# Optimization experiments

Measured on AMD Instinct MI355X. Metric: run time of the kernel, lower is better.

Reference implementation:

```python
import jax, jax.numpy as jnp
import numpy as np

N = 50000   # nodes
E = 1600000 # edges
C = 32      # all channel dims


def _p(k, shape):
    return jax.random.normal(k, shape, dtype=jnp.float32) * 0.05


def setup_inputs() -> dict:
    key = jax.random.key(0)
    ks = jax.random.split(key, 32)
    inp = {
        "node_attr": jax.random.normal(ks[0], (N, C), dtype=jnp.float32),
        "edge_attr": jax.random.normal(ks[1], (E, C), dtype=jnp.float32),
        "edge_index": jax.random.randint(ks[2], (2, E), 0, N, dtype=jnp.int32),
        # conv1: in = 2*32 + 32 = 96
        "c1w1": _p(ks[3], (96, C)),  "c1b1": jnp.zeros((C,), jnp.float32),
        "c1w2": _p(ks[4], (C, C)),   "c1b2": jnp.zeros((C,), jnp.float32),
        # conv2: in = 2*32 + 64 = 128
        "c2w1": _p(ks[5], (128, C)), "c2b1": jnp.zeros((C,), jnp.float32),
        "c2w2": _p(ks[6], (C, C)),   "c2b2": jnp.zeros((C,), jnp.float32),
        # conv3: in = 2*32 + 96 = 160
        "c3w1": _p(ks[7], (160, C)), "c3b1": jnp.zeros((C,), jnp.float32),
        "c3w2": _p(ks[8], (C, C)),   "c3b2": jnp.zeros((C,), jnp.float32),
        # node_out_mlp: three 32->32 linears
        "nw1": _p(ks[9], (C, C)),  "nb1": jnp.zeros((C,), jnp.float32),
        "nw2": _p(ks[10], (C, C)), "nb2": jnp.zeros((C,), jnp.float32),
        "nw3": _p(ks[11], (C, C)), "nb3": jnp.zeros((C,), jnp.float32),
        # edge_out_mlp: three 32->32 linears
        "ew1": _p(ks[12], (C, C)), "eb1": jnp.zeros((C,), jnp.float32),
        "ew2": _p(ks[13], (C, C)), "eb2": jnp.zeros((C,), jnp.float32),
        "ew3": _p(ks[14], (C, C)), "eb3": jnp.zeros((C,), jnp.float32),
    }
    return inp


def _lrelu(x):
    return jnp.where(x > 0, x, 0.2 * x)


def _edge_conv(x, row, col, ea, w1, b1, w2, b2):
    # gather endpoints, concat with edge features, 2-layer MLP on edges
    h = jnp.concatenate([x[row], x[col], ea], axis=1)        # [E, 2C + ce]
    edge_out = jax.nn.relu(h @ w1 + b1) @ w2 + b2            # [E, C]
    # scatter-mean back to source nodes (zero-degree nodes -> 0)
    n = x.shape[0]
    s = jax.ops.segment_sum(edge_out, row, num_segments=n)
    cnt = jax.ops.segment_sum(jnp.ones((edge_out.shape[0], 1), edge_out.dtype), row, num_segments=n)
    node_out = s / jnp.maximum(cnt, 1.0)
    return node_out, edge_out


def reference(node_attr, edge_attr, edge_index,
              c1w1, c1b1, c1w2, c1b2,
              c2w1, c2b1, c2w2, c2b2,
              c3w1, c3b1, c3w2, c3b2,
              nw1, nb1, nw2, nb2, nw3, nb3,
              ew1, eb1, ew2, eb2, ew3, eb3):
    row, col = edge_index[0], edge_index[1]

    n1, e1 = _edge_conv(node_attr, row, col, edge_attr, c1w1, c1b1, c1w2, c1b2)
    n1, e1 = _lrelu(n1), _lrelu(e1)

    n2, e2 = _edge_conv(n1, row, col, jnp.concatenate([e1, edge_attr], axis=-1),
                        c2w1, c2b1, c2w2, c2b2)
    n2, e2 = _lrelu(n2), _lrelu(e2)

    n3, e3 = _edge_conv(n2, row, col, jnp.concatenate([e2, e1, edge_attr], axis=-1),
                        c3w1, c3b1, c3w2, c3b2)
    n3, e3 = _lrelu(n3), _lrelu(e3)

    node_out = _lrelu(_lrelu(n3 @ nw1 + nb1) @ nw2 + nb2) @ nw3 + nb3
    edge_out = _lrelu(_lrelu(e3 @ ew1 + eb1) @ ew2 + eb2) @ ew3 + eb3
    return node_out, edge_out
```

## Files before the change

### kernel.cpp

```cpp
#include <hip/hip_runtime.h>

#define DEVINL __device__ __forceinline__

constexpr int PADF = 36;

DEVINL float lrelu1(float v)    { return v > 0.f ? v : 0.2f * v; }
DEVINL float invlrelu1(float v) { return v > 0.f ? v : 5.0f * v; }

DEVINL void gemm_block(const float* __restrict__ wg, const float* hrow, float acc[32])
{
#pragma unroll
    for (int cb = 0; cb < 4; ++cb) {
#pragma unroll 1
        for (int kq = 0; kq < 8; ++kq) {
            float4 h = *(const float4*)(hrow + kq * 4);
#pragma unroll
            for (int i = 0; i < 4; ++i) {
                float hv = ((const float*)&h)[i];
                float w8[8];
                *(float4*)&w8[0] = *(const float4*)(wg + (kq * 4 + i) * 32 + cb * 8);
                *(float4*)&w8[4] = *(const float4*)(wg + (kq * 4 + i) * 32 + cb * 8 + 4);
#pragma unroll
                for (int jj = 0; jj < 8; ++jj)
                    acc[cb * 8 + jj] = fmaf(hv, w8[jj], acc[cb * 8 + jj]);
            }
        }
    }
}

DEVINL void stage_rows(const float* __restrict__ src, float* __restrict__ hs,
                       int base, int se, int sq, int limit)
{
#pragma unroll
    for (int p = 0; p < 8; ++p) {
        int lr = p * 32 + se;
        int m = base + lr; if (m >= limit) m = limit - 1;
        float4 v = *(const float4*)(src + (size_t)m * 32 + sq * 4);
        *(float4*)&hs[lr * PADF + sq * 4] = v;
    }
}

__global__ __launch_bounds__(256)
void hist_kernel(const int* __restrict__ rowi, int* __restrict__ deg, int E)
{
    int e = blockIdx.x * 256 + threadIdx.x;
    if (e < E) atomicAdd(&deg[rowi[e]], 1);
}

__global__ __launch_bounds__(256)
void scan_kernel(const int* __restrict__ deg, int* __restrict__ off,
                 int* __restrict__ cursor, int N, int E)
{
    __shared__ int part[256];
    __shared__ int psum[256];
    const int t = threadIdx.x;
    const int per = (N + 255) / 256;
    const int b0 = t * per;
    int s = 0;
    for (int i = 0; i < per; ++i) { int idx = b0 + i; if (idx < N) s += deg[idx]; }
    part[t] = s;
    __syncthreads();
    if (t == 0) { int run = 0; for (int i = 0; i < 256; ++i) { psum[i] = run; run += part[i]; } }
    __syncthreads();
    int run = psum[t];
    for (int i = 0; i < per; ++i) {
        int idx = b0 + i;
        if (idx < N) { off[idx] = run; cursor[idx] = run; run += deg[idx]; }
    }
    if (t == 0) off[N] = E;
}

__global__ __launch_bounds__(256)
void place_kernel(const int* __restrict__ rowi, int* __restrict__ cursor,
                  int* __restrict__ perm, int E)
{
    int e = blockIdx.x * 256 + threadIdx.x;
    if (e < E) {
        int r = rowi[e];
        int p = atomicAdd(&cursor[r], 1);
        perm[p] = e;
    }
}

__global__ __launch_bounds__(256, 4)
void pre_kernel(const float* __restrict__ x, const float* __restrict__ w1,
                const float* __restrict__ b1,
                float* __restrict__ Pr, float* __restrict__ Pc, int N)
{
    __shared__ float hs[256 * PADF];
    const int tid = threadIdx.x;
    const int base = blockIdx.x * 256;
    const int se = tid >> 3, sq = tid & 7;
    const float* hrow = hs + tid * PADF;

    stage_rows(x, hs, base, se, sq, N);
    __syncthreads();

    const int n = base + tid;
    float acc[32];
#pragma unroll
    for (int j = 0; j < 32; ++j) acc[j] = b1[j];
    gemm_block(w1, hrow, acc);
    if (n < N) {
#pragma unroll
        for (int j = 0; j < 32; j += 4)
            *(float4*)(Pr + (size_t)n * 32 + j) = make_float4(acc[j], acc[j+1], acc[j+2], acc[j+3]);
    }
#pragma unroll
    for (int j = 0; j < 32; ++j) acc[j] = 0.f;
    gemm_block(w1 + 1024, hrow, acc);
    if (n < N) {
#pragma unroll
        for (int j = 0; j < 32; j += 4)
            *(float4*)(Pc + (size_t)n * 32 + j) = make_float4(acc[j], acc[j+1], acc[j+2], acc[j+3]);
    }
}

template<int NCHUNK, bool FUSE>
__global__ __launch_bounds__(256, 4)
void conv_kernel(const float* __restrict__ Pr, const float* __restrict__ Pc,
                 const int* __restrict__ rowi, const int* __restrict__ coli,
                 const float* __restrict__ f0, const float* __restrict__ f1,
                 const float* __restrict__ f2,
                 const float* __restrict__ w1e,
                 const float* __restrict__ w2g, const float* __restrict__ b2g,
                 float* __restrict__ eout,
                 const float* __restrict__ mw1, const float* __restrict__ mb1,
                 const float* __restrict__ mw2, const float* __restrict__ mb2,
                 const float* __restrict__ mw3, const float* __restrict__ mb3,
                 float* __restrict__ mout,
                 int E)
{
    __shared__ float hs[256 * PADF];
    const int tid = threadIdx.x;
    const int base = blockIdx.x * 256;
    const int se = tid >> 3, sq = tid & 7;
    float* hrow = hs + tid * PADF;

    stage_rows(f0, hs, base, se, sq, E);

    const int e = base + tid;
    const int ee = e < E ? e : E - 1;
    const int r = rowi[ee], c = coli[ee];
    const float* pr = Pr + (size_t)r * 32;
    const float* pc = Pc + (size_t)c * 32;
    float4 ga[8], gb[8];
#pragma unroll
    for (int q = 0; q < 8; ++q) ga[q] = *(const float4*)(pr + q * 4);
#pragma unroll
    for (int q = 0; q < 8; ++q) gb[q] = *(const float4*)(pc + q * 4);
    float acc[32];
#pragma unroll
    for (int q = 0; q < 8; ++q) {
        acc[q * 4 + 0] = ga[q].x + gb[q].x;
        acc[q * 4 + 1] = ga[q].y + gb[q].y;
        acc[q * 4 + 2] = ga[q].z + gb[q].z;
        acc[q * 4 + 3] = ga[q].w + gb[q].w;
    }

    __syncthreads();
    gemm_block(w1e, hrow, acc);
#pragma unroll
    for (int cch = 1; cch < NCHUNK; ++cch) {
        const float* src = (cch == 1) ? f1 : f2;
        __syncthreads();
        stage_rows(src, hs, base, se, sq, E);
        __syncthreads();
        gemm_block(w1e + cch * 1024, hrow, acc);
    }

#pragma unroll
    for (int j = 0; j < 32; j += 4) {
        float4 v;
        v.x = fmaxf(acc[j],     0.f); v.y = fmaxf(acc[j + 1], 0.f);
        v.z = fmaxf(acc[j + 2], 0.f); v.w = fmaxf(acc[j + 3], 0.f);
        *(float4*)&hrow[j] = v;
    }
    float acc2[32];
#pragma unroll
    for (int j = 0; j < 32; ++j) acc2[j] = b2g[j];
    gemm_block(w2g, hrow, acc2);

    if constexpr (!FUSE) {
        if (e < E) {
#pragma unroll
            for (int j = 0; j < 32; j += 4) {
                float4 v;
                v.x = lrelu1(acc2[j]);     v.y = lrelu1(acc2[j + 1]);
                v.z = lrelu1(acc2[j + 2]); v.w = lrelu1(acc2[j + 3]);
                *(float4*)(eout + (size_t)e * 32 + j) = v;
            }
        }
    } else {
#pragma unroll
        for (int j = 0; j < 32; j += 4) {
            float4 v;
            v.x = lrelu1(acc2[j]);     v.y = lrelu1(acc2[j + 1]);
            v.z = lrelu1(acc2[j + 2]); v.w = lrelu1(acc2[j + 3]);
            *(float4*)&hrow[j] = v;
            if (e < E) *(float4*)(eout + (size_t)e * 32 + j) = v;
        }
        float acc3[32];
#pragma unroll
        for (int j = 0; j < 32; ++j) acc3[j] = mb1[j];
        gemm_block(mw1, hrow, acc3);
#pragma unroll
        for (int j = 0; j < 32; j += 4) {
            float4 v;
            v.x = lrelu1(acc3[j]);     v.y = lrelu1(acc3[j + 1]);
            v.z = lrelu1(acc3[j + 2]); v.w = lrelu1(acc3[j + 3]);
            *(float4*)&hrow[j] = v;
        }
#pragma unroll
        for (int j = 0; j < 32; ++j) acc3[j] = mb2[j];
        gemm_block(mw2, hrow, acc3);
#pragma unroll
        for (int j = 0; j < 32; j += 4) {
            float4 v;
            v.x = lrelu1(acc3[j]);     v.y = lrelu1(acc3[j + 1]);
            v.z = lrelu1(acc3[j + 2]); v.w = lrelu1(acc3[j + 3]);
            *(float4*)&hrow[j] = v;
        }
#pragma unroll
        for (int j = 0; j < 32; ++j) acc3[j] = mb3[j];
        gemm_block(mw3, hrow, acc3);
        if (e < E) {
#pragma unroll
            for (int j = 0; j < 32; j += 4)
                *(float4*)(mout + (size_t)e * 32 + j) =
                    make_float4(acc3[j], acc3[j + 1], acc3[j + 2], acc3[j + 3]);
        }
    }
}

__global__ __launch_bounds__(256)
void mean_kernel(const float* __restrict__ esrc, const int* __restrict__ off,
                 const int* __restrict__ perm, float* __restrict__ nout, int N)
{
    const int t = threadIdx.x;
    const int n = blockIdx.x * 32 + (t >> 3);
    if (n >= N) return;
    const int cg = t & 7;
    const int o0 = off[n], o1 = off[n + 1];
    float4 acc = make_float4(0.f, 0.f, 0.f, 0.f);
    for (int i = o0; i < o1; ++i) {
        int e = perm[i];
        float4 v = *(const float4*)(esrc + (size_t)e * 32 + cg * 4);
        acc.x += invlrelu1(v.x); acc.y += invlrelu1(v.y);
        acc.z += invlrelu1(v.z); acc.w += invlrelu1(v.w);
    }
    float inv = 1.0f / (float)max(o1 - o0, 1);
    float4 r;
    r.x = lrelu1(acc.x * inv); r.y = lrelu1(acc.y * inv);
    r.z = lrelu1(acc.z * inv); r.w = lrelu1(acc.w * inv);
    *(float4*)(nout + (size_t)n * 32 + cg * 4) = r;
}

__global__ __launch_bounds__(256, 4)
void mlp3_kernel(const float* __restrict__ in,
                 const float* __restrict__ w1g, const float* __restrict__ b1g,
                 const float* __restrict__ w2g, const float* __restrict__ b2g,
                 const float* __restrict__ w3g, const float* __restrict__ b3g,
                 float* __restrict__ out, int M)
{
    __shared__ float hs[256 * PADF];
    const int tid = threadIdx.x;
    const int base = blockIdx.x * 256;
    const int se = tid >> 3, sq = tid & 7;
    float* hrow = hs + tid * PADF;

    stage_rows(in, hs, base, se, sq, M);
    __syncthreads();

    float acc[32];
#pragma unroll
    for (int j = 0; j < 32; ++j) acc[j] = b1g[j];
    gemm_block(w1g, hrow, acc);
#pragma unroll
    for (int j = 0; j < 32; j += 4) {
        float4 v;
        v.x = lrelu1(acc[j]);     v.y = lrelu1(acc[j + 1]);
        v.z = lrelu1(acc[j + 2]); v.w = lrelu1(acc[j + 3]);
        *(float4*)&hrow[j] = v;
    }
#pragma unroll
    for (int j = 0; j < 32; ++j) acc[j] = b2g[j];
    gemm_block(w2g, hrow, acc);
#pragma unroll
    for (int j = 0; j < 32; j += 4) {
        float4 v;
        v.x = lrelu1(acc[j]);     v.y = lrelu1(acc[j + 1]);
        v.z = lrelu1(acc[j + 2]); v.w = lrelu1(acc[j + 3]);
        *(float4*)&hrow[j] = v;
    }
#pragma unroll
    for (int j = 0; j < 32; ++j) acc[j] = b3g[j];
    gemm_block(w3g, hrow, acc);

    int m = base + tid;
    if (m < M) {
#pragma unroll
        for (int j = 0; j < 32; j += 4)
            *(float4*)(out + (size_t)m * 32 + j) =
                make_float4(acc[j], acc[j + 1], acc[j + 2], acc[j + 3]);
    }
}

extern "C" void kernel_launch(void* const* d_in, const int* in_sizes, int n_in,
                              void* d_out, int out_size, void* d_ws, size_t ws_size,
                              hipStream_t stream)
{
    const float* node_attr = (const float*)d_in[0];
    const float* edge_attr = (const float*)d_in[1];
    const int*   eidx      = (const int*)d_in[2];
    const float* c1w1 = (const float*)d_in[3];  const float* c1b1 = (const float*)d_in[4];
    const float* c1w2 = (const float*)d_in[5];  const float* c1b2 = (const float*)d_in[6];
    const float* c2w1 = (const float*)d_in[7];  const float* c2b1 = (const float*)d_in[8];
    const float* c2w2 = (const float*)d_in[9];  const float* c2b2 = (const float*)d_in[10];
    const float* c3w1 = (const float*)d_in[11]; const float* c3b1 = (const float*)d_in[12];
    const float* c3w2 = (const float*)d_in[13]; const float* c3b2 = (const float*)d_in[14];
    const float* nw1  = (const float*)d_in[15]; const float* nb1  = (const float*)d_in[16];
    const float* nw2  = (const float*)d_in[17]; const float* nb2  = (const float*)d_in[18];
    const float* nw3  = (const float*)d_in[19]; const float* nb3  = (const float*)d_in[20];
    const float* ew1  = (const float*)d_in[21]; const float* eb1  = (const float*)d_in[22];
    const float* ew2  = (const float*)d_in[23]; const float* eb2  = (const float*)d_in[24];
    const float* ew3  = (const float*)d_in[25]; const float* eb3  = (const float*)d_in[26];

    const int N = in_sizes[0] / 32;
    const int E = in_sizes[1] / 32;
    const int* rowi = eidx;
    const int* coli = eidx + E;

    float* out      = (float*)d_out;
    float* node_out = out;
    float* edge_out = out + (size_t)N * 32;

    int* deg    = (int*)d_ws;
    int* off    = deg + N;
    int* cursor = off + (N + 1);
    int* perm   = cursor + N;
    uintptr_t a = ((uintptr_t)(perm + E) + 255) & ~(uintptr_t)255;
    float* n1 = (float*)a;
    float* n2 = n1 + (size_t)32 * N;
    float* e1 = n2 + (size_t)32 * N;
    float* e2 = e1 + (size_t)32 * E;

    const int gridE   = (E + 255) / 256;
    const int gridN32 = (N + 31) / 32;
    const int gridN   = (N + 255) / 256;

    hipMemsetAsync(deg, 0, (size_t)N * sizeof(int), stream);
    hist_kernel<<<gridE, 256, 0, stream>>>(rowi, deg, E);
    scan_kernel<<<1, 256, 0, stream>>>(deg, off, cursor, N, E);
    place_kernel<<<gridE, 256, 0, stream>>>(rowi, cursor, perm, E);

    pre_kernel<<<gridN, 256, 0, stream>>>(node_attr, c1w1, c1b1, n1, n2, N);
    conv_kernel<1, false><<<gridE, 256, 0, stream>>>(
        n1, n2, rowi, coli, edge_attr, nullptr, nullptr,
        c1w1 + 2048, c1w2, c1b2, e1,
        nullptr, nullptr, nullptr, nullptr, nullptr, nullptr, nullptr, E);
    mean_kernel<<<gridN32, 256, 0, stream>>>(e1, off, perm, n1, N);

    pre_kernel<<<gridN, 256, 0, stream>>>(n1, c2w1, c2b1, n1, n2, N);
    conv_kernel<2, false><<<gridE, 256, 0, stream>>>(
        n1, n2, rowi, coli, e1, edge_attr, nullptr,
        c2w1 + 2048, c2w2, c2b2, e2,
        nullptr, nullptr, nullptr, nullptr, nullptr, nullptr, nullptr, E);
    mean_kernel<<<gridN32, 256, 0, stream>>>(e2, off, perm, n2, N);

    pre_kernel<<<gridN, 256, 0, stream>>>(n2, c3w1, c3b1, n2, n1, N);
    conv_kernel<3, true><<<gridE, 256, 0, stream>>>(
        n2, n1, rowi, coli, e2, e1, edge_attr,
        c3w1 + 2048, c3w2, c3b2,  e1,
        ew1, eb1, ew2, eb2, ew3, eb3,  edge_out, E);
    mean_kernel<<<gridN32, 256, 0, stream>>>(e1, off, perm, n1, N);

    mlp3_kernel<<<gridN, 256, 0, stream>>>(n1, nw1, nb1, nw2, nb2, nw3, nb3,
                                           node_out, N);
}
```

Before: 1.728 ms.

## Prefetch next edge feature chunk into registers during GEMM and restructure inner loop

Splits shared-memory staging into separate global-load and LDS-write steps, so the next feature chunk is loaded into registers while the current chunk's GEMM runs. This hides global load latency behind compute in the edge kernel. The gemm inner loop is also restructured to walk all 32 output columns per input element and to prefetch the next h float4 one step ahead. The trade-off is extra register pressure (32 staging floats), which may lower occupancy under the launch bounds.

```diff
diff --git a/kernel.cpp b/kernel.cpp
--- a/kernel.cpp
+++ b/kernel.cpp
@@ -9,35 +9,42 @@
 
 DEVINL void gemm_block(const float* __restrict__ wg, const float* hrow, float acc[32])
 {
-#pragma unroll
-    for (int cb = 0; cb < 4; ++cb) {
+    float4 h = *(const float4*)(hrow);
 #pragma unroll 1
-        for (int kq = 0; kq < 8; ++kq) {
-            float4 h = *(const float4*)(hrow + kq * 4);
-#pragma unroll
-            for (int i = 0; i < 4; ++i) {
-                float hv = ((const float*)&h)[i];
-                float w8[8];
-                *(float4*)&w8[0] = *(const float4*)(wg + (kq * 4 + i) * 32 + cb * 8);
-                *(float4*)&w8[4] = *(const float4*)(wg + (kq * 4 + i) * 32 + cb * 8 + 4);
-#pragma unroll
-                for (int jj = 0; jj < 8; ++jj)
-                    acc[cb * 8 + jj] = fmaf(hv, w8[jj], acc[cb * 8 + jj]);
+    for (int kq = 0; kq < 8; ++kq) {
+        float4 hn = *(const float4*)(hrow + ((kq + 1) & 7) * 4);
+#pragma unroll
+        for (int i = 0; i < 4; ++i) {
+            float hv = ((const float*)&h)[i];
+            const float* wr = wg + (kq * 4 + i) * 32;
+#pragma unroll
+            for (int j = 0; j < 32; j += 4) {
+                float4 w = *(const float4*)(wr + j);
+                acc[j + 0] = fmaf(hv, w.x, acc[j + 0]);
+                acc[j + 1] = fmaf(hv, w.y, acc[j + 1]);
+                acc[j + 2] = fmaf(hv, w.z, acc[j + 2]);
+                acc[j + 3] = fmaf(hv, w.w, acc[j + 3]);
             }
         }
-    }
-}
-
-DEVINL void stage_rows(const float* __restrict__ src, float* __restrict__ hs,
+        h = hn;
+    }
+}
+
+DEVINL void stage_load(const float* __restrict__ src, float4 stg[8],
                        int base, int se, int sq, int limit)
 {
 #pragma unroll
     for (int p = 0; p < 8; ++p) {
-        int lr = p * 32 + se;
-        int m = base + lr; if (m >= limit) m = limit - 1;
-        float4 v = *(const float4*)(src + (size_t)m * 32 + sq * 4);
-        *(float4*)&hs[lr * PADF + sq * 4] = v;
-    }
+        int m = base + p * 32 + se; if (m >= limit) m = limit - 1;
+        stg[p] = *(const float4*)(src + (size_t)m * 32 + sq * 4);
+    }
+}
+
+DEVINL void stage_write(const float4 stg[8], float* __restrict__ hs, int se, int sq)
+{
+#pragma unroll
+    for (int p = 0; p < 8; ++p)
+        *(float4*)&hs[(p * 32 + se) * PADF + sq * 4] = stg[p];
 }
 
 __global__ __launch_bounds__(256)
@@ -93,7 +100,9 @@
     const int se = tid >> 3, sq = tid & 7;
     const float* hrow = hs + tid * PADF;
 
-    stage_rows(x, hs, base, se, sq, N);
+    float4 stg[8];
+    stage_load(x, stg, base, se, sq, N);
+    stage_write(stg, hs, se, sq);
     __syncthreads();
 
     const int n = base + tid;
@@ -137,36 +146,39 @@
     const int se = tid >> 3, sq = tid & 7;
     float* hrow = hs + tid * PADF;
 
-    stage_rows(f0, hs, base, se, sq, E);
+    float4 stg[8];
+    stage_load(f0, stg, base, se, sq, E);
 
     const int e = base + tid;
     const int ee = e < E ? e : E - 1;
     const int r = rowi[ee], c = coli[ee];
     const float* pr = Pr + (size_t)r * 32;
     const float* pc = Pc + (size_t)c * 32;
-    float4 ga[8], gb[8];
-#pragma unroll
-    for (int q = 0; q < 8; ++q) ga[q] = *(const float4*)(pr + q * 4);
-#pragma unroll
-    for (int q = 0; q < 8; ++q) gb[q] = *(const float4*)(pc + q * 4);
     float acc[32];
 #pragma unroll
     for (int q = 0; q < 8; ++q) {
-        acc[q * 4 + 0] = ga[q].x + gb[q].x;
-        acc[q * 4 + 1] = ga[q].y + gb[q].y;
-        acc[q * 4 + 2] = ga[q].z + gb[q].z;
-        acc[q * 4 + 3] = ga[q].w + gb[q].w;
-    }
-
-    __syncthreads();
-    gemm_block(w1e, hrow, acc);
-#pragma unroll
-    for (int cch = 1; cch < NCHUNK; ++cch) {
-        const float* src = (cch == 1) ? f1 : f2;
-        __syncthreads();
-        stage_rows(src, hs, base, se, sq, E);
-        __syncthreads();
+        float4 ga = *(const float4*)(pr + q * 4);
+        float4 gb = *(const float4*)(pc + q * 4);
+        acc[q * 4 + 0] = ga.x + gb.x;
+        acc[q * 4 + 1] = ga.y + gb.y;
+        acc[q * 4 + 2] = ga.z + gb.z;
+        acc[q * 4 + 3] = ga.w + gb.w;
+    }
+    stage_write(stg, hs, se, sq);
+    __syncthreads();
+
+#pragma unroll
+    for (int cch = 0; cch < NCHUNK; ++cch) {
+        if (cch + 1 < NCHUNK) {
+            const float* src = (cch == 0) ? f1 : f2;
+            stage_load(src, stg, base, se, sq, E);
+        }
         gemm_block(w1e + cch * 1024, hrow, acc);
+        if (cch + 1 < NCHUNK) {
+            __syncthreads();
+            stage_write(stg, hs, se, sq);
+            __syncthreads();
+        }
     }
 
 #pragma unroll
@@ -269,7 +281,9 @@
     const int se = tid >> 3, sq = tid & 7;
     float* hrow = hs + tid * PADF;
 
-    stage_rows(in, hs, base, se, sq, M);
+    float4 stg[8];
+    stage_load(in, stg, base, se, sq, M);
+    stage_write(stg, hs, se, sq);
     __syncthreads();
 
     float acc[32];
```

New measurement: 1.851 ms. 7.1% more time.
